# Kernel tuning notes

Measured on AMD Instinct MI355X. Metric: run time of the kernel, lower is better.

The kernel has to match this reference:

```python
import jax, jax.numpy as jnp
import numpy as np

B, T, D, H, L, V = 16, 1024, 512, 8, 6, 96
HS = D // H
FF = 4 * D


def setup_inputs() -> dict:
    key = jax.random.key(0)
    ks = jax.random.split(key, 16)
    n = lambda k, shape: jax.random.normal(k, shape, jnp.float32) * 0.02
    return {
        "idx": jax.random.randint(ks[0], (B, T), 0, V),
        "targets": jax.random.randint(ks[1], (B, T), 0, V),
        "tok_emb": n(ks[2], (V, D)),
        "pos_emb": n(ks[3], (T, D)),
        "Wq": n(ks[4], (L, H, D, HS)),
        "Wk": n(ks[5], (L, H, D, HS)),
        "Wv": n(ks[6], (L, H, D, HS)),
        "Wproj": n(ks[7], (L, D, D)),
        "bproj": jnp.zeros((L, D), jnp.float32),
        "W1": n(ks[8], (L, D, FF)),
        "b1": jnp.zeros((L, FF), jnp.float32),
        "W2": n(ks[9], (L, FF, D)),
        "b2": jnp.zeros((L, D), jnp.float32),
        "ln1_s": jnp.ones((L, D), jnp.float32),
        "ln1_b": jnp.zeros((L, D), jnp.float32),
        "ln2_s": jnp.ones((L, D), jnp.float32),
        "ln2_b": jnp.zeros((L, D), jnp.float32),
        "lnf_s": jnp.ones((D,), jnp.float32),
        "lnf_b": jnp.zeros((D,), jnp.float32),
        "Wout": n(ks[10], (D, V)),
        "bout": jnp.zeros((V,), jnp.float32),
    }


def _ln(x, s, b, eps=1e-5):
    m = x.mean(-1, keepdims=True)
    v = ((x - m) ** 2).mean(-1, keepdims=True)
    return (x - m) * jax.lax.rsqrt(v + eps) * s + b


def reference(idx, targets, tok_emb, pos_emb, Wq, Wk, Wv, Wproj, bproj,
              W1, b1, W2, b2, ln1_s, ln1_b, ln2_s, ln2_b, lnf_s, lnf_b,
              Wout, bout):
    x = tok_emb[idx] + pos_emb[:T]  # [B,T,D]
    causal = jnp.tril(jnp.ones((T, T), jnp.bool_))
    scale = D ** (-0.5)  # NOTE: source scales by full channel dim, not head_size
    for l in range(L):
        h = _ln(x, ln1_s[l], ln1_b[l])
        q = jnp.einsum("btd,hdk->bhtk", h, Wq[l])
        k = jnp.einsum("btd,hdk->bhtk", h, Wk[l])
        v = jnp.einsum("btd,hdk->bhtk", h, Wv[l])
        att = jnp.einsum("bhtk,bhsk->bhts", q, k) * scale
        att = jnp.where(causal, att, -jnp.inf)
        att = jax.nn.softmax(att, axis=-1)
        o = jnp.einsum("bhts,bhsk->bhtk", att, v)
        o = o.transpose(0, 2, 1, 3).reshape(B, T, D)  # concat heads
        x = x + (o @ Wproj[l] + bproj[l])
        h2 = _ln(x, ln2_s[l], ln2_b[l])
        x = x + (jnp.maximum(h2 @ W1[l] + b1[l], 0.0) @ W2[l] + b2[l])
    x = _ln(x, lnf_s, lnf_b)
    logits = (x @ Wout + bout).reshape(B * T, V)
    logp = jax.nn.log_softmax(logits, axis=-1)
    loss = -logp[jnp.arange(B * T), targets.reshape(-1)].mean()
    return logits, loss
```

## Files before the change

### kernel.cpp

```cpp
#include <hip/hip_runtime.h>

#define B_  16
#define T_  1024
#define D_  512
#define H_  8
#define L_  6
#define V_  96
#define HS_ 64
#define FF_ 2048
#define BT_ (B_*T_)
#define QKS 1024

typedef __attribute__((ext_vector_type(8))) short bf16x8;
typedef __attribute__((ext_vector_type(4))) float f32x4;

typedef __attribute__((address_space(3))) unsigned int lds_u32_t;
typedef const __attribute__((address_space(1))) unsigned int glb_u32_t;

__device__ __forceinline__ void gload16(const unsigned short* g, unsigned short* l) {
  __builtin_amdgcn_global_load_lds((glb_u32_t*)g, (lds_u32_t*)l, 16, 0, 0);
}

__device__ __forceinline__ unsigned short f2b(float f) {
  unsigned u = __float_as_uint(f);
  unsigned r = (u + 0x7FFFu + ((u >> 16) & 1u)) >> 16;
  return (unsigned short)r;
}

__global__ void zero_kernel(float* p) { p[0] = 0.f; }

__global__ __launch_bounds__(128) void embed_kernel(const int* __restrict__ idx,
    const float* __restrict__ tok, const float* __restrict__ pos, float* __restrict__ x) {
  int bt = blockIdx.x;
  int t  = bt & (T_ - 1);
  int id = idx[bt];
  if (id < 0) id = 0; if (id > V_ - 1) id = V_ - 1;
  int d  = threadIdx.x * 4;
  float4 tv = *(const float4*)(tok + (size_t)id * D_ + d);
  float4 pv = *(const float4*)(pos + (size_t)t  * D_ + d);
  float4 o = {tv.x + pv.x, tv.y + pv.y, tv.z + pv.z, tv.w + pv.w};
  *(float4*)(x + (size_t)bt * D_ + d) = o;
}

__global__ __launch_bounds__(256) void transpose_cvt(const float* __restrict__ src,
    unsigned short* __restrict__ dst, int R, int C, long sstride, long dstride,
    int zper, long zouter) {
  __shared__ float t[32][33];
  const float* s = src + (size_t)blockIdx.z * sstride;
  unsigned short* d = dst + (size_t)(blockIdx.z / zper) * zouter
                          + (size_t)(blockIdx.z % zper) * dstride;
  int r0 = blockIdx.y * 32, c0 = blockIdx.x * 32;
  int tr = threadIdx.x >> 5, tc = threadIdx.x & 31;
#pragma unroll
  for (int i = 0; i < 4; ++i)
    t[tr + i * 8][tc] = s[(size_t)(r0 + tr + i * 8) * C + c0 + tc];
  __syncthreads();
#pragma unroll
  for (int i = 0; i < 4; ++i)
    d[(size_t)(c0 + tr + i * 8) * R + r0 + tc] = f2b(t[tc][tr + i * 8]);
}

template<bool BF16OUT>
__global__ __launch_bounds__(256) void ln_kernel(const float* __restrict__ x,
    const float* __restrict__ s, const float* __restrict__ b, void* __restrict__ outv) {
  int wave = threadIdx.x >> 6;
  int lane = threadIdx.x & 63;
  int r = blockIdx.x * 4 + wave;
  const float* xr = x + (size_t)r * D_;
  float vals[8];
  float sum = 0.f;
#pragma unroll
  for (int j = 0; j < 8; ++j) { vals[j] = xr[j * 64 + lane]; sum += vals[j]; }
#pragma unroll
  for (int o = 32; o > 0; o >>= 1) sum += __shfl_xor(sum, o, 64);
  float mean = sum * (1.f / D_);
  float vs = 0.f;
#pragma unroll
  for (int j = 0; j < 8; ++j) { float d = vals[j] - mean; vs += d * d; }
#pragma unroll
  for (int o = 32; o > 0; o >>= 1) vs += __shfl_xor(vs, o, 64);
  float rstd = rsqrtf(vs * (1.f / D_) + 1e-5f);
#pragma unroll
  for (int j = 0; j < 8; ++j) {
    int c = j * 64 + lane;
    float v = (vals[j] - mean) * rstd * s[c] + b[c];
    if (BF16OUT) ((unsigned short*)outv)[(size_t)r * D_ + c] = f2b(v);
    else         ((float*)outv)[(size_t)r * D_ + c] = v;
  }
}

#define BK 32
template<bool ACC, bool RELU, bool BIAS, int OUTMODE>
__global__ __launch_bounds__(256) void mfma_gemm(
    const unsigned short* __restrict__ A,
    const unsigned short* __restrict__ Bt,
    const float* __restrict__ bias,
    void* __restrict__ Cv, void* __restrict__ Cv2,
    int K, int ldc) {
  __shared__ unsigned short Al[2][128 * BK];
  __shared__ unsigned short Bl[2][128 * BK];
  const int m0 = blockIdx.x * 128, n0 = blockIdx.y * 128;
  const int tid = threadIdx.x;
  const int lane = tid & 63, wave = tid >> 6;
  const int wy = wave >> 1, wx = wave & 1;
  const int l15 = lane & 15, quad = lane >> 4;

  const int sbase = wave * 1024;
  const int soff  = sbase + lane * 16;
  const int r0 = soff >> 6, c0e = (soff & 63) >> 1;
  const int r1 = r0 + 64;
  const int ls = sbase >> 1;
  const unsigned short* gA0 = A  + (size_t)(m0 + r0) * K + c0e;
  const unsigned short* gA1 = A  + (size_t)(m0 + r1) * K + c0e;
  const unsigned short* gB0 = Bt + (size_t)(n0 + r0) * K + c0e;
  const unsigned short* gB1 = Bt + (size_t)(n0 + r1) * K + c0e;

  f32x4 acc[4][4];
  const f32x4 z4 = {0.f, 0.f, 0.f, 0.f};
#pragma unroll
  for (int mi = 0; mi < 4; ++mi)
#pragma unroll
    for (int ni = 0; ni < 4; ++ni) acc[mi][ni] = z4;

  gload16(gA0, &Al[0][ls]);
  gload16(gA1, &Al[0][ls + 2048]);
  gload16(gB0, &Bl[0][ls]);
  gload16(gB1, &Bl[0][ls + 2048]);
  __syncthreads();

  const int nsteps = K / BK;
  int cur = 0;
  for (int s = 0; s < nsteps; ++s) {
    if (s + 1 < nsteps) {
      const int k0 = (s + 1) * BK;
      gload16(gA0 + k0, &Al[cur ^ 1][ls]);
      gload16(gA1 + k0, &Al[cur ^ 1][ls + 2048]);
      gload16(gB0 + k0, &Bl[cur ^ 1][ls]);
      gload16(gB1 + k0, &Bl[cur ^ 1][ls + 2048]);
    }
    bf16x8 af[4], bfr[4];
#pragma unroll
    for (int mi = 0; mi < 4; ++mi)
      af[mi] = *(const bf16x8*)(&Al[cur][(wy * 64 + mi * 16 + l15) * BK + quad * 8]);
#pragma unroll
    for (int ni = 0; ni < 4; ++ni)
      bfr[ni] = *(const bf16x8*)(&Bl[cur][(wx * 64 + ni * 16 + l15) * BK + quad * 8]);
#pragma unroll
    for (int mi = 0; mi < 4; ++mi)
#pragma unroll
      for (int ni = 0; ni < 4; ++ni)
        acc[mi][ni] = __builtin_amdgcn_mfma_f32_16x16x32_bf16(af[mi], bfr[ni], acc[mi][ni], 0, 0, 0);
    if (s + 1 < nsteps) {
      __syncthreads();
      cur ^= 1;
    }
  }

#pragma unroll
  for (int mi = 0; mi < 4; ++mi) {
    int row0 = m0 + wy * 64 + mi * 16 + quad * 4;
#pragma unroll
    for (int ni = 0; ni < 4; ++ni) {
      int col = n0 + wx * 64 + ni * 16 + l15;
      float bb = BIAS ? bias[col] : 0.f;
#pragma unroll
      for (int r = 0; r < 4; ++r) {
        float v = acc[mi][ni][r] + bb;
        if (RELU) v = fmaxf(v, 0.f);
        int row = row0 + r;
        if (OUTMODE == 3) {
          if (col < 1024) {
            ((unsigned short*)Cv)[(size_t)row * QKS + col] = f2b(v);
          } else {
            int vcol = col - 1024;
            int b = row >> 10, t = row & (T_ - 1);
            int h = vcol >> 6, hs = vcol & 63;
            ((unsigned short*)Cv2)[((size_t)((b * H_ + h) * HS_ + hs)) * T_ + t] = f2b(v);
          }
        } else {
          size_t off = (size_t)row * ldc + col;
          if (ACC) v += ((const float*)Cv)[off];
          if (OUTMODE == 1) ((unsigned short*)Cv)[off] = f2b(v);
          else              ((float*)Cv)[off] = v;
        }
      }
    }
  }
}

#define PSTR 72
__global__ __launch_bounds__(256) void attn_mfma(const unsigned short* __restrict__ q,
    const unsigned short* __restrict__ k, const unsigned short* __restrict__ vt,
    unsigned short* __restrict__ o) {
  __shared__ unsigned short Pbuf[2][64 * PSTR];
  __shared__ float Lsum[4][64];
  const int qt = (gridDim.x - 1) - blockIdx.x;
  const int bh = blockIdx.y;
  const int b = bh >> 3, hh = bh & 7;
  const int tid = threadIdx.x;
  const int lane = tid & 63, w = tid >> 6;
  const int l15 = lane & 15, quad = lane >> 4;
  const float CEXP = 0.044194173824159216f * 1.4426950408889634f;

  bf16x8 qf[4][2];
#pragma unroll
  for (int mi = 0; mi < 4; ++mi)
#pragma unroll
    for (int c = 0; c < 2; ++c)
      qf[mi][c] = *(const bf16x8*)(q + (size_t)(b * T_ + qt * 64 + mi * 16 + l15) * QKS
                                     + hh * HS_ + c * 32 + quad * 8);

  f32x4 oacc[4];
  float psum[4][4];
  const f32x4 z4 = {0.f, 0.f, 0.f, 0.f};
#pragma unroll
  for (int mi = 0; mi < 4; ++mi) {
    oacc[mi] = z4;
#pragma unroll
    for (int r = 0; r < 4; ++r) psum[mi][r] = 0.f;
  }

  const unsigned short* kbase = k  + (size_t)(b * T_ + w * 16 + l15) * QKS + hh * HS_ + quad * 8;
  const unsigned short* vbase = vt + ((size_t)(bh * HS_ + w * 16 + l15)) * T_ + quad * 8;

  bf16x8 kf[2], vf[2];
#pragma unroll
  for (int c = 0; c < 2; ++c) {
    kf[c] = *(const bf16x8*)(kbase + c * 32);
    vf[c] = *(const bf16x8*)(vbase + c * 32);
  }

  const int gc = w * 16 + l15;

  for (int kt = 0; kt <= qt; ++kt) {
    const int ktn = (kt < qt) ? kt + 1 : qt;
    bf16x8 kfn[2], vfn[2];
#pragma unroll
    for (int c = 0; c < 2; ++c) {
      kfn[c] = *(const bf16x8*)(kbase + (size_t)ktn * 64 * QKS + c * 32);
      vfn[c] = *(const bf16x8*)(vbase + ktn * 64 + c * 32);
    }

    f32x4 s[4];
#pragma unroll
    for (int mi = 0; mi < 4; ++mi) s[mi] = z4;
    __builtin_amdgcn_s_setprio(1);
#pragma unroll
    for (int c = 0; c < 2; ++c)
#pragma unroll
      for (int mi = 0; mi < 4; ++mi)
        s[mi] = __builtin_amdgcn_mfma_f32_16x16x32_bf16(qf[mi][c], kf[c], s[mi], 0, 0, 0);
    __builtin_amdgcn_s_setprio(0);

    unsigned short* pb = Pbuf[kt & 1];
    if (kt == qt) {
#pragma unroll
      for (int mi = 0; mi < 4; ++mi)
#pragma unroll
        for (int r = 0; r < 4; ++r) {
          int row = mi * 16 + quad * 4 + r;
          float p = (gc > row) ? 0.f : exp2f(s[mi][r] * CEXP);
          unsigned short us = f2b(p);
          psum[mi][r] += __uint_as_float((unsigned)us << 16);
          pb[row * PSTR + gc] = us;
        }
    } else {
#pragma unroll
      for (int mi = 0; mi < 4; ++mi)
#pragma unroll
        for (int r = 0; r < 4; ++r) {
          int row = mi * 16 + quad * 4 + r;
          float p = exp2f(s[mi][r] * CEXP);
          unsigned short us = f2b(p);
          psum[mi][r] += __uint_as_float((unsigned)us << 16);
          pb[row * PSTR + gc] = us;
        }
    }
    __syncthreads();
    __builtin_amdgcn_s_setprio(1);
#pragma unroll
    for (int c = 0; c < 2; ++c) {
#pragma unroll
      for (int mi = 0; mi < 4; ++mi) {
        bf16x8 pf = *(const bf16x8*)(&pb[(mi * 16 + l15) * PSTR + c * 32 + quad * 8]);
        oacc[mi] = __builtin_amdgcn_mfma_f32_16x16x32_bf16(pf, vf[c], oacc[mi], 0, 0, 0);
      }
    }
    __builtin_amdgcn_s_setprio(0);
#pragma unroll
    for (int c = 0; c < 2; ++c) { kf[c] = kfn[c]; vf[c] = vfn[c]; }
  }

#pragma unroll
  for (int mi = 0; mi < 4; ++mi)
#pragma unroll
    for (int r = 0; r < 4; ++r) {
#pragma unroll
      for (int off = 1; off < 16; off <<= 1)
        psum[mi][r] += __shfl_xor(psum[mi][r], off, 64);
    }
  if (l15 == 0) {
#pragma unroll
    for (int mi = 0; mi < 4; ++mi)
#pragma unroll
      for (int r = 0; r < 4; ++r)
        Lsum[w][mi * 16 + quad * 4 + r] = psum[mi][r];
  }
  __syncthreads();
#pragma unroll
  for (int mi = 0; mi < 4; ++mi)
#pragma unroll
    for (int r = 0; r < 4; ++r) {
      int row = mi * 16 + quad * 4 + r;
      float inv = 1.f / (Lsum[0][row] + Lsum[1][row] + Lsum[2][row] + Lsum[3][row]);
      o[(size_t)(b * T_ + qt * 64 + row) * D_ + hh * HS_ + w * 16 + l15] =
          f2b(oacc[mi][r] * inv);
    }
}

__global__ __launch_bounds__(256) void gemm_f32_kernel(const float* __restrict__ A, int lda,
    const float* __restrict__ Bw, int ldb, const float* __restrict__ bias,
    float* __restrict__ C, int ldc, int K, int N) {
  __shared__ float As[16][64];
  __shared__ float Bs[16][64];
  int n0 = blockIdx.y * 64;
  int nv = N - n0; if (nv > 64) nv = 64;
  int m0 = blockIdx.x * 64;
  const int tid = threadIdx.x;
  const int tx = tid & 15, ty = tid >> 4;
  const int amm = tid >> 2;
  const int akk = (tid & 3) * 4;
  const int bkk = tid >> 4;
  const int bnn = (tid & 15) * 4;
  float acc[4][4] = {};
  for (int k0 = 0; k0 < K; k0 += 16) {
    float4 av = *(const float4*)(A + (size_t)(m0 + amm) * lda + k0 + akk);
    As[akk + 0][amm] = av.x; As[akk + 1][amm] = av.y;
    As[akk + 2][amm] = av.z; As[akk + 3][amm] = av.w;
    if (bnn < nv) {
      float4 bv = *(const float4*)(Bw + (size_t)(k0 + bkk) * ldb + n0 + bnn);
      Bs[bkk][bnn + 0] = bv.x; Bs[bkk][bnn + 1] = bv.y;
      Bs[bkk][bnn + 2] = bv.z; Bs[bkk][bnn + 3] = bv.w;
    } else {
      Bs[bkk][bnn + 0] = 0.f; Bs[bkk][bnn + 1] = 0.f;
      Bs[bkk][bnn + 2] = 0.f; Bs[bkk][bnn + 3] = 0.f;
    }
    __syncthreads();
#pragma unroll
    for (int kk = 0; kk < 16; ++kk) {
      float4 a4 = *(const float4*)(&As[kk][ty * 4]);
      float4 b4 = *(const float4*)(&Bs[kk][tx * 4]);
      float aa[4] = {a4.x, a4.y, a4.z, a4.w};
      float bb[4] = {b4.x, b4.y, b4.z, b4.w};
#pragma unroll
      for (int i = 0; i < 4; ++i)
#pragma unroll
        for (int j = 0; j < 4; ++j)
          acc[i][j] = fmaf(aa[i], bb[j], acc[i][j]);
    }
    __syncthreads();
  }
  if (tx * 4 < nv) {
#pragma unroll
    for (int i = 0; i < 4; ++i) {
      float* cp = C + (size_t)(m0 + ty * 4 + i) * ldc + n0 + tx * 4;
      float4 st = {acc[i][0] + bias[n0 + tx * 4 + 0], acc[i][1] + bias[n0 + tx * 4 + 1],
                   acc[i][2] + bias[n0 + tx * 4 + 2], acc[i][3] + bias[n0 + tx * 4 + 3]};
      *(float4*)cp = st;
    }
  }
}

__global__ __launch_bounds__(256) void loss_kernel(const float* __restrict__ logits,
    const int* __restrict__ targets, float* __restrict__ loss_acc) {
  __shared__ float wsum[4];
  int wave = threadIdx.x >> 6, lane = threadIdx.x & 63;
  float local = 0.f;
  for (int r = blockIdx.x * 4 + wave; r < BT_; r += gridDim.x * 4) {
    const float* lr = logits + (size_t)r * V_;
    float v0 = lr[lane];
    float v1 = (lane < 32) ? lr[64 + lane] : -INFINITY;
    float mx = fmaxf(v0, v1);
#pragma unroll
    for (int o = 32; o > 0; o >>= 1) mx = fmaxf(mx, __shfl_xor(mx, o, 64));
    float se = expf(v0 - mx) + ((lane < 32) ? expf(v1 - mx) : 0.f);
#pragma unroll
    for (int o = 32; o > 0; o >>= 1) se += __shfl_xor(se, o, 64);
    if (lane == 0) {
      int tg = targets[r];
      if (tg < 0) tg = 0; if (tg > V_ - 1) tg = V_ - 1;
      local += (mx + logf(se)) - lr[tg];
    }
  }
  if (lane == 0) wsum[wave] = local;
  __syncthreads();
  if (threadIdx.x == 0)
    atomicAdd(loss_acc, wsum[0] + wsum[1] + wsum[2] + wsum[3]);
}

__global__ void loss_finalize_kernel(const float* __restrict__ acc, float* __restrict__ out) {
  out[(size_t)BT_ * V_] = acc[0] * (1.f / BT_);
}

static void* g_ws_fallback = nullptr;

extern "C" void kernel_launch(void* const* d_in, const int* in_sizes, int n_in,
                              void* d_out, int out_size, void* d_ws, size_t ws_size,
                              hipStream_t stream) {
  const int*   idx     = (const int*)d_in[0];
  const int*   targets = (const int*)d_in[1];
  const float* tok  = (const float*)d_in[2];
  const float* pos  = (const float*)d_in[3];
  const float* Wq   = (const float*)d_in[4];
  const float* Wk   = (const float*)d_in[5];
  const float* Wv   = (const float*)d_in[6];
  const float* Wp   = (const float*)d_in[7];
  const float* bp   = (const float*)d_in[8];
  const float* W1   = (const float*)d_in[9];
  const float* b1   = (const float*)d_in[10];
  const float* W2   = (const float*)d_in[11];
  const float* b2   = (const float*)d_in[12];
  const float* l1s  = (const float*)d_in[13];
  const float* l1b  = (const float*)d_in[14];
  const float* l2s  = (const float*)d_in[15];
  const float* l2b  = (const float*)d_in[16];
  const float* lfs  = (const float*)d_in[17];
  const float* lfb  = (const float*)d_in[18];
  const float* Wout = (const float*)d_in[19];
  const float* bout = (const float*)d_in[20];
  float* out = (float*)d_out;

  const size_t n_x  = (size_t)BT_ * D_;
  const size_t n_wT = 9437184;
  const size_t need_floats = n_x + n_x + n_x / 2 + n_x / 2 + n_x / 2 +
                             (size_t)BT_ * FF_ / 2 + n_wT + 256;
  const size_t need_bytes  = need_floats * sizeof(float);

  float* ws;
  if (ws_size >= need_bytes) {
    ws = (float*)d_ws;
  } else {
    if (!g_ws_fallback) (void)hipMalloc(&g_ws_fallback, need_bytes);
    ws = (float*)g_ws_fallback;
  }

  size_t off = 0;
  float* x  = ws + off; off += n_x;
  float* qf32 = ws + off; off += n_x;
  unsigned short* qkb = (unsigned short*)qf32;
  unsigned short* spare = (unsigned short*)(ws + off); off += n_x / 2;
  unsigned short* vtb = (unsigned short*)(ws + off); off += n_x / 2;
  unsigned short* hb  = (unsigned short*)(ws + off); off += n_x / 2;
  unsigned short* ffb = (unsigned short*)(ws + off); off += (size_t)BT_ * FF_ / 2;
  unsigned short* wqkvT = (unsigned short*)(ws + off);
  unsigned short* wpT = wqkvT + (size_t)L_ * 3 * D_ * D_;
  unsigned short* w1T = wpT + (size_t)L_ * D_ * D_;
  unsigned short* w2T = w1T + (size_t)L_ * D_ * FF_;
  off += n_wT;
  float* lacc = ws + off;
  (void)spare;

  const long DD = (long)D_ * D_;
  const long L3DD = 3 * DD;

  zero_kernel<<<1, 1, 0, stream>>>(lacc);
  embed_kernel<<<BT_, 128, 0, stream>>>(idx, tok, pos, x);

  transpose_cvt<<<dim3(2, 16, 48), 256, 0, stream>>>(Wq, wqkvT,            512, 64, 32768, 32768, 8, L3DD);
  transpose_cvt<<<dim3(2, 16, 48), 256, 0, stream>>>(Wk, wqkvT + DD,       512, 64, 32768, 32768, 8, L3DD);
  transpose_cvt<<<dim3(2, 16, 48), 256, 0, stream>>>(Wv, wqkvT + 2 * DD,   512, 64, 32768, 32768, 8, L3DD);
  transpose_cvt<<<dim3(16, 16, 6), 256, 0, stream>>>(Wp, wpT, 512, 512, 262144, 0, 1, 262144);
  transpose_cvt<<<dim3(64, 16, 6), 256, 0, stream>>>(W1, w1T, 512, 2048, 1048576, 0, 1, 1048576);
  transpose_cvt<<<dim3(16, 64, 6), 256, 0, stream>>>(W2, w2T, 2048, 512, 1048576, 0, 1, 1048576);

  const dim3 gQKV(BT_ / 128, 12);
  const dim3 gD(BT_ / 128, D_ / 128);
  const dim3 gF(BT_ / 128, FF_ / 128);

  for (int l = 0; l < L_; ++l) {
    ln_kernel<true><<<BT_ / 4, 256, 0, stream>>>(x, l1s + (size_t)l * D_, l1b + (size_t)l * D_, hb);
    mfma_gemm<false, false, false, 3><<<gQKV, 256, 0, stream>>>(
        hb, wqkvT + (size_t)l * L3DD, nullptr, qkb, vtb, D_, 0);
    attn_mfma<<<dim3(T_ / 64, B_ * H_), 256, 0, stream>>>(qkb, qkb + 512, vtb, hb);
    mfma_gemm<true, false, true, 0><<<gD, 256, 0, stream>>>(
        hb, wpT + (size_t)l * DD, bp + (size_t)l * D_, x, nullptr, D_, D_);
    ln_kernel<true><<<BT_ / 4, 256, 0, stream>>>(x, l2s + (size_t)l * D_, l2b + (size_t)l * D_, hb);
    mfma_gemm<false, true, true, 1><<<gF, 256, 0, stream>>>(
        hb, w1T + (size_t)l * D_ * FF_, b1 + (size_t)l * FF_, ffb, nullptr, D_, FF_);
    mfma_gemm<true, false, true, 0><<<gD, 256, 0, stream>>>(
        ffb, w2T + (size_t)l * FF_ * D_, b2 + (size_t)l * D_, x, nullptr, FF_, D_);
  }

  ln_kernel<false><<<BT_ / 4, 256, 0, stream>>>(x, lfs, lfb, qf32);
  gemm_f32_kernel<<<dim3(BT_ / 64, 2), 256, 0, stream>>>(
      qf32, D_, Wout, V_, bout, out, V_, D_, V_);
  loss_kernel<<<64, 256, 0, stream>>>(out, targets, lacc);
  loss_finalize_kernel<<<1, 1, 0, stream>>>(lacc, out);
}
```

Measured before the change: 2.065 ms.

## Pair causal attention tiles per block and use 64-row tiles for narrow GEMMs

```diff
diff --git a/kernel.cpp b/kernel.cpp
--- a/kernel.cpp
+++ b/kernel.cpp
@@ -90,19 +90,22 @@
 }
 
 #define BK 32
-template<bool ACC, bool RELU, bool BIAS, int OUTMODE>
+template<bool ACC, bool RELU, bool BIAS, int OUTMODE, int MT>
 __global__ __launch_bounds__(256) void mfma_gemm(
     const unsigned short* __restrict__ A,
     const unsigned short* __restrict__ Bt,
     const float* __restrict__ bias,
     void* __restrict__ Cv, void* __restrict__ Cv2,
     int K, int ldc) {
-  __shared__ unsigned short Al[2][128 * BK];
+  constexpr int NI = (MT == 128) ? 4 : 2;
+  constexpr int WN = (MT == 128) ? 64 : 32;
+  __shared__ unsigned short Al[2][MT * BK];
   __shared__ unsigned short Bl[2][128 * BK];
-  const int m0 = blockIdx.x * 128, n0 = blockIdx.y * 128;
+  const int m0 = blockIdx.x * MT, n0 = blockIdx.y * 128;
   const int tid = threadIdx.x;
   const int lane = tid & 63, wave = tid >> 6;
-  const int wy = wave >> 1, wx = wave & 1;
+  const int wy = (MT == 128) ? (wave >> 1) : 0;
+  const int wx = (MT == 128) ? (wave & 1) : wave;
   const int l15 = lane & 15, quad = lane >> 4;
 
   const int sbase = wave * 1024;
@@ -115,40 +118,38 @@
   const unsigned short* gB0 = Bt + (size_t)(n0 + r0) * K + c0e;
   const unsigned short* gB1 = Bt + (size_t)(n0 + r1) * K + c0e;
 
-  f32x4 acc[4][4];
+  auto stage = [&](int buf, int k0) {
+    gload16(gA0 + k0, &Al[buf][ls]);
+    if constexpr (MT == 128) gload16(gA1 + k0, &Al[buf][ls + 2048]);
+    gload16(gB0 + k0, &Bl[buf][ls]);
+    gload16(gB1 + k0, &Bl[buf][ls + 2048]);
+  };
+
+  f32x4 acc[4][NI];
   const f32x4 z4 = {0.f, 0.f, 0.f, 0.f};
 #pragma unroll
   for (int mi = 0; mi < 4; ++mi)
 #pragma unroll
-    for (int ni = 0; ni < 4; ++ni) acc[mi][ni] = z4;
-
-  gload16(gA0, &Al[0][ls]);
-  gload16(gA1, &Al[0][ls + 2048]);
-  gload16(gB0, &Bl[0][ls]);
-  gload16(gB1, &Bl[0][ls + 2048]);
+    for (int ni = 0; ni < NI; ++ni) acc[mi][ni] = z4;
+
+  stage(0, 0);
   __syncthreads();
 
   const int nsteps = K / BK;
   int cur = 0;
   for (int s = 0; s < nsteps; ++s) {
-    if (s + 1 < nsteps) {
-      const int k0 = (s + 1) * BK;
-      gload16(gA0 + k0, &Al[cur ^ 1][ls]);
-      gload16(gA1 + k0, &Al[cur ^ 1][ls + 2048]);
-      gload16(gB0 + k0, &Bl[cur ^ 1][ls]);
-      gload16(gB1 + k0, &Bl[cur ^ 1][ls + 2048]);
-    }
-    bf16x8 af[4], bfr[4];
+    if (s + 1 < nsteps) stage(cur ^ 1, (s + 1) * BK);
+    bf16x8 af[4], bfr[NI];
 #pragma unroll
     for (int mi = 0; mi < 4; ++mi)
       af[mi] = *(const bf16x8*)(&Al[cur][(wy * 64 + mi * 16 + l15) * BK + quad * 8]);
 #pragma unroll
-    for (int ni = 0; ni < 4; ++ni)
-      bfr[ni] = *(const bf16x8*)(&Bl[cur][(wx * 64 + ni * 16 + l15) * BK + quad * 8]);
+    for (int ni = 0; ni < NI; ++ni)
+      bfr[ni] = *(const bf16x8*)(&Bl[cur][(wx * WN + ni * 16 + l15) * BK + quad * 8]);
 #pragma unroll
     for (int mi = 0; mi < 4; ++mi)
 #pragma unroll
-      for (int ni = 0; ni < 4; ++ni)
+      for (int ni = 0; ni < NI; ++ni)
         acc[mi][ni] = __builtin_amdgcn_mfma_f32_16x16x32_bf16(af[mi], bfr[ni], acc[mi][ni], 0, 0, 0);
     if (s + 1 < nsteps) {
       __syncthreads();
@@ -160,8 +161,8 @@
   for (int mi = 0; mi < 4; ++mi) {
     int row0 = m0 + wy * 64 + mi * 16 + quad * 4;
 #pragma unroll
-    for (int ni = 0; ni < 4; ++ni) {
-      int col = n0 + wx * 64 + ni * 16 + l15;
+    for (int ni = 0; ni < NI; ++ni) {
+      int col = n0 + wx * WN + ni * 16 + l15;
       float bb = BIAS ? bias[col] : 0.f;
 #pragma unroll
       for (int r = 0; r < 4; ++r) {
@@ -194,7 +195,6 @@
     unsigned short* __restrict__ o) {
   __shared__ unsigned short Pbuf[2][64 * PSTR];
   __shared__ float Lsum[4][64];
-  const int qt = (gridDim.x - 1) - blockIdx.x;
   const int bh = blockIdx.y;
   const int b = bh >> 3, hh = bh & 7;
   const int tid = threadIdx.x;
@@ -202,120 +202,123 @@
   const int l15 = lane & 15, quad = lane >> 4;
   const float CEXP = 0.044194173824159216f * 1.4426950408889634f;
 
-  bf16x8 qf[4][2];
-#pragma unroll
-  for (int mi = 0; mi < 4; ++mi)
-#pragma unroll
-    for (int c = 0; c < 2; ++c)
-      qf[mi][c] = *(const bf16x8*)(q + (size_t)(b * T_ + qt * 64 + mi * 16 + l15) * QKS
-                                     + hh * HS_ + c * 32 + quad * 8);
-
-  f32x4 oacc[4];
-  float psum[4][4];
-  const f32x4 z4 = {0.f, 0.f, 0.f, 0.f};
-#pragma unroll
-  for (int mi = 0; mi < 4; ++mi) {
-    oacc[mi] = z4;
-#pragma unroll
-    for (int r = 0; r < 4; ++r) psum[mi][r] = 0.f;
-  }
-
   const unsigned short* kbase = k  + (size_t)(b * T_ + w * 16 + l15) * QKS + hh * HS_ + quad * 8;
   const unsigned short* vbase = vt + ((size_t)(bh * HS_ + w * 16 + l15)) * T_ + quad * 8;
-
-  bf16x8 kf[2], vf[2];
-#pragma unroll
-  for (int c = 0; c < 2; ++c) {
-    kf[c] = *(const bf16x8*)(kbase + c * 32);
-    vf[c] = *(const bf16x8*)(vbase + c * 32);
-  }
-
   const int gc = w * 16 + l15;
-
-  for (int kt = 0; kt <= qt; ++kt) {
-    const int ktn = (kt < qt) ? kt + 1 : qt;
-    bf16x8 kfn[2], vfn[2];
+  const f32x4 z4 = {0.f, 0.f, 0.f, 0.f};
+
+  for (int pass = 0; pass < 2; ++pass) {
+    const int qt = pass ? (int)blockIdx.x : (T_ / 64 - 1 - (int)blockIdx.x);
+
+    bf16x8 qf[4][2];
+#pragma unroll
+    for (int mi = 0; mi < 4; ++mi)
+#pragma unroll
+      for (int c = 0; c < 2; ++c)
+        qf[mi][c] = *(const bf16x8*)(q + (size_t)(b * T_ + qt * 64 + mi * 16 + l15) * QKS
+                                       + hh * HS_ + c * 32 + quad * 8);
+
+    f32x4 oacc[4];
+    float psum[4][4];
+#pragma unroll
+    for (int mi = 0; mi < 4; ++mi) {
+      oacc[mi] = z4;
+#pragma unroll
+      for (int r = 0; r < 4; ++r) psum[mi][r] = 0.f;
+    }
+
+    bf16x8 kf[2], vf[2];
 #pragma unroll
     for (int c = 0; c < 2; ++c) {
-      kfn[c] = *(const bf16x8*)(kbase + (size_t)ktn * 64 * QKS + c * 32);
-      vfn[c] = *(const bf16x8*)(vbase + ktn * 64 + c * 32);
-    }
-
-    f32x4 s[4];
-#pragma unroll
-    for (int mi = 0; mi < 4; ++mi) s[mi] = z4;
-    __builtin_amdgcn_s_setprio(1);
-#pragma unroll
-    for (int c = 0; c < 2; ++c)
+      kf[c] = *(const bf16x8*)(kbase + c * 32);
+      vf[c] = *(const bf16x8*)(vbase + c * 32);
+    }
+
+    for (int kt = 0; kt <= qt; ++kt) {
+      const int ktn = (kt < qt) ? kt + 1 : qt;
+      bf16x8 kfn[2], vfn[2];
+#pragma unroll
+      for (int c = 0; c < 2; ++c) {
+        kfn[c] = *(const bf16x8*)(kbase + (size_t)ktn * 64 * QKS + c * 32);
+        vfn[c] = *(const bf16x8*)(vbase + ktn * 64 + c * 32);
+      }
+
+      f32x4 s[4];
+#pragma unroll
+      for (int mi = 0; mi < 4; ++mi) s[mi] = z4;
+      __builtin_amdgcn_s_setprio(1);
+#pragma unroll
+      for (int c = 0; c < 2; ++c)
+#pragma unroll
+        for (int mi = 0; mi < 4; ++mi)
+          s[mi] = __builtin_amdgcn_mfma_f32_16x16x32_bf16(qf[mi][c], kf[c], s[mi], 0, 0, 0);
+      __builtin_amdgcn_s_setprio(0);
+
+      unsigned short* pb = Pbuf[kt & 1];
+      if (kt == qt) {
+#pragma unroll
+        for (int mi = 0; mi < 4; ++mi)
+#pragma unroll
+          for (int r = 0; r < 4; ++r) {
+            int row = mi * 16 + quad * 4 + r;
+            float p = (gc > row) ? 0.f : exp2f(s[mi][r] * CEXP);
+            unsigned short us = f2b(p);
+            psum[mi][r] += __uint_as_float((unsigned)us << 16);
+            pb[row * PSTR + gc] = us;
+          }
+      } else {
+#pragma unroll
+        for (int mi = 0; mi < 4; ++mi)
+#pragma unroll
+          for (int r = 0; r < 4; ++r) {
+            int row = mi * 16 + quad * 4 + r;
+            float p = exp2f(s[mi][r] * CEXP);
+            unsigned short us = f2b(p);
+            psum[mi][r] += __uint_as_float((unsigned)us << 16);
+            pb[row * PSTR + gc] = us;
+          }
+      }
+      __syncthreads();
+      __builtin_amdgcn_s_setprio(1);
+#pragma unroll
+      for (int c = 0; c < 2; ++c) {
+#pragma unroll
+        for (int mi = 0; mi < 4; ++mi) {
+          bf16x8 pf = *(const bf16x8*)(&pb[(mi * 16 + l15) * PSTR + c * 32 + quad * 8]);
+          oacc[mi] = __builtin_amdgcn_mfma_f32_16x16x32_bf16(pf, vf[c], oacc[mi], 0, 0, 0);
+        }
+      }
+      __builtin_amdgcn_s_setprio(0);
+#pragma unroll
+      for (int c = 0; c < 2; ++c) { kf[c] = kfn[c]; vf[c] = vfn[c]; }
+    }
+
+#pragma unroll
+    for (int mi = 0; mi < 4; ++mi)
+#pragma unroll
+      for (int r = 0; r < 4; ++r) {
+#pragma unroll
+        for (int off = 1; off < 16; off <<= 1)
+          psum[mi][r] += __shfl_xor(psum[mi][r], off, 64);
+      }
+    if (l15 == 0) {
 #pragma unroll
       for (int mi = 0; mi < 4; ++mi)
-        s[mi] = __builtin_amdgcn_mfma_f32_16x16x32_bf16(qf[mi][c], kf[c], s[mi], 0, 0, 0);
-    __builtin_amdgcn_s_setprio(0);
-
-    unsigned short* pb = Pbuf[kt & 1];
-    if (kt == qt) {
-#pragma unroll
-      for (int mi = 0; mi < 4; ++mi)
-#pragma unroll
-        for (int r = 0; r < 4; ++r) {
-          int row = mi * 16 + quad * 4 + r;
-          float p = (gc > row) ? 0.f : exp2f(s[mi][r] * CEXP);
-          unsigned short us = f2b(p);
-          psum[mi][r] += __uint_as_float((unsigned)us << 16);
-          pb[row * PSTR + gc] = us;
-        }
-    } else {
-#pragma unroll
-      for (int mi = 0; mi < 4; ++mi)
-#pragma unroll
-        for (int r = 0; r < 4; ++r) {
-          int row = mi * 16 + quad * 4 + r;
-          float p = exp2f(s[mi][r] * CEXP);
-          unsigned short us = f2b(p);
-          psum[mi][r] += __uint_as_float((unsigned)us << 16);
-          pb[row * PSTR + gc] = us;
-        }
+#pragma unroll
+        for (int r = 0; r < 4; ++r)
+          Lsum[w][mi * 16 + quad * 4 + r] = psum[mi][r];
     }
     __syncthreads();
-    __builtin_amdgcn_s_setprio(1);
-#pragma unroll
-    for (int c = 0; c < 2; ++c) {
-#pragma unroll
-      for (int mi = 0; mi < 4; ++mi) {
-        bf16x8 pf = *(const bf16x8*)(&pb[(mi * 16 + l15) * PSTR + c * 32 + quad * 8]);
-        oacc[mi] = __builtin_amdgcn_mfma_f32_16x16x32_bf16(pf, vf[c], oacc[mi], 0, 0, 0);
+#pragma unroll
+    for (int mi = 0; mi < 4; ++mi)
+#pragma unroll
+      for (int r = 0; r < 4; ++r) {
+        int row = mi * 16 + quad * 4 + r;
+        float inv = 1.f / (Lsum[0][row] + Lsum[1][row] + Lsum[2][row] + Lsum[3][row]);
+        o[(size_t)(b * T_ + qt * 64 + row) * D_ + hh * HS_ + w * 16 + l15] =
+            f2b(oacc[mi][r] * inv);
       }
-    }
-    __builtin_amdgcn_s_setprio(0);
-#pragma unroll
-    for (int c = 0; c < 2; ++c) { kf[c] = kfn[c]; vf[c] = vfn[c]; }
-  }
-
-#pragma unroll
-  for (int mi = 0; mi < 4; ++mi)
-#pragma unroll
-    for (int r = 0; r < 4; ++r) {
-#pragma unroll
-      for (int off = 1; off < 16; off <<= 1)
-        psum[mi][r] += __shfl_xor(psum[mi][r], off, 64);
-    }
-  if (l15 == 0) {
-#pragma unroll
-    for (int mi = 0; mi < 4; ++mi)
-#pragma unroll
-      for (int r = 0; r < 4; ++r)
-        Lsum[w][mi * 16 + quad * 4 + r] = psum[mi][r];
-  }
-  __syncthreads();
-#pragma unroll
-  for (int mi = 0; mi < 4; ++mi)
-#pragma unroll
-    for (int r = 0; r < 4; ++r) {
-      int row = mi * 16 + quad * 4 + r;
-      float inv = 1.f / (Lsum[0][row] + Lsum[1][row] + Lsum[2][row] + Lsum[3][row]);
-      o[(size_t)(b * T_ + qt * 64 + row) * D_ + hh * HS_ + w * 16 + l15] =
-          f2b(oacc[mi][r] * inv);
-    }
+  }
 }
 
 __global__ __launch_bounds__(256) void gemm_f32_kernel(const float* __restrict__ A, int lda,
@@ -474,20 +477,20 @@
   transpose_cvt<<<dim3(16, 64, 6), 256, 0, stream>>>(W2, w2T, 2048, 512, 1048576, 0, 1, 1048576);
 
   const dim3 gQKV(BT_ / 128, 12);
-  const dim3 gD(BT_ / 128, D_ / 128);
+  const dim3 gD64(BT_ / 64, D_ / 128);
   const dim3 gF(BT_ / 128, FF_ / 128);
 
   for (int l = 0; l < L_; ++l) {
     ln_kernel<true><<<BT_ / 4, 256, 0, stream>>>(x, l1s + (size_t)l * D_, l1b + (size_t)l * D_, hb);
-    mfma_gemm<false, false, false, 3><<<gQKV, 256, 0, stream>>>(
+    mfma_gemm<false, false, false, 3, 128><<<gQKV, 256, 0, stream>>>(
         hb, wqkvT + (size_t)l * L3DD, nullptr, qkb, vtb, D_, 0);
-    attn_mfma<<<dim3(T_ / 64, B_ * H_), 256, 0, stream>>>(qkb, qkb + 512, vtb, hb);
-    mfma_gemm<true, false, true, 0><<<gD, 256, 0, stream>>>(
+    attn_mfma<<<dim3(T_ / 128, B_ * H_), 256, 0, stream>>>(qkb, qkb + 512, vtb, hb);
+    mfma_gemm<true, false, true, 0, 64><<<gD64, 256, 0, stream>>>(
         hb, wpT + (size_t)l * DD, bp + (size_t)l * D_, x, nullptr, D_, D_);
     ln_kernel<true><<<BT_ / 4, 256, 0, stream>>>(x, l2s + (size_t)l * D_, l2b + (size_t)l * D_, hb);
-    mfma_gemm<false, true, true, 1><<<gF, 256, 0, stream>>>(
+    mfma_gemm<false, true, true, 1, 128><<<gF, 256, 0, stream>>>(
         hb, w1T + (size_t)l * D_ * FF_, b1 + (size_t)l * FF_, ffb, nullptr, D_, FF_);
-    mfma_gemm<true, false, true, 0><<<gD, 256, 0, stream>>>(
+    mfma_gemm<true, false, true, 0, 64><<<gD64, 256, 0, stream>>>(
         ffb, w2T + (size_t)l * FF_ * D_, b2 + (size_t)l * D_, x, nullptr, FF_, D_);
   }
 
```

After: 1.881 ms. -8.9%, faster.
